# Kernel optimization log

Hardware: AMD Instinct MI355X
Metric: run time of the kernel (lower is better)

## Reference

```python
import jax, jax.numpy as jnp
import numpy as np

# Model hyperparameters (from __init__)
SIGMA = 0.2
LAMBDA_0 = 1.0
LAMBDA_INF = 0.1
LAMBDA_DECAY = 0.01
MU_J = 0.0
SIGMA_J = 0.3
TOTAL_STEPS = 10000
KAPPA = float(np.exp(MU_J + 0.5 * SIGMA_J ** 2) - 1.0)  # E[e^Y - 1]

# Simulation dims (simulate_path args)
T_TOTAL = 1.0
N_STEPS = 2048
N_PATHS = 32768
DT = T_TOTAL / N_STEPS


def _jump_intensity(t):
    # lambda(t) = lambda_inf + (lambda_0 - lambda_inf) * exp(-decay * t)
    # (t/total_steps * total_steps cancels in the original code)
    return LAMBDA_INF + (LAMBDA_0 - LAMBDA_INF) * jnp.exp(-LAMBDA_DECAY * t)


def setup_inputs() -> dict:
    key = jax.random.key(0)
    k1, k2, k3 = jax.random.split(key, 3)
    # Per-step time-varying Poisson rate for jump counts
    t = jnp.arange(N_STEPS, dtype=jnp.float32) * DT  # (n_steps,)
    lam_dt = _jump_intensity(t) * DT                  # (n_steps,)
    n_jumps = jax.random.poisson(k3, lam_dt[:, None], shape=(N_STEPS, N_PATHS)).astype(jnp.int32)
    return {
        "S0": jnp.ones((1,), dtype=jnp.float32),                         # initial price
        "z_diff": jax.random.normal(k1, (N_STEPS, N_PATHS), jnp.float32),  # Brownian increments / sqrt(dt)
        "z_jump": jax.random.normal(k2, (N_STEPS, N_PATHS), jnp.float32),  # jump-sum normals
        "n_jumps": n_jumps,                                              # Poisson jump counts
    }


def reference(S0, z_diff, z_jump, n_jumps):
    dtype = z_diff.dtype
    t = jnp.arange(N_STEPS, dtype=dtype) * DT          # (n_steps,)
    lam = _jump_intensity(t)[:, None]                   # (n_steps, 1)
    # Sum of n_jumps iid N(mu_J, sigma_J^2) jumps == N(n*mu_J, n*sigma_J^2)
    nj = n_jumps.astype(dtype)
    jump_sizes = nj * MU_J + jnp.sqrt(nj) * SIGMA_J * z_jump
    drift = (0.0 - lam * KAPPA) * DT
    diffusion = SIGMA * jnp.asarray(np.sqrt(DT), dtype) * z_diff
    log_ret = drift + diffusion + jump_sizes            # (n_steps, n_paths)
    log_paths = jnp.cumsum(log_ret, axis=0)             # (n_steps, n_paths)
    log_paths = jnp.concatenate([jnp.zeros((1, log_ret.shape[1]), dtype), log_paths], axis=0)
    paths = (S0[0] * jnp.exp(log_paths)).T              # (n_paths, n_steps + 1)
    return paths
```

## Files before the change

kernel.cpp:

```cpp
#include <hip/hip_runtime.h>
#include <math.h>


#define N_STEPS 2048
#define N_PATHS 32768
#define U 16
#define TILE_S 64
#define ROW (N_STEPS + 1)

#define DT_F 0.00048828125f
#define C_DIFF_F 0.004419417382415922f
#define KAPPA_F 0.046027859908717f

__device__ __forceinline__ void load_batch(const float* __restrict__ zd_p,
                                           const float* __restrict__ zj_p,
                                           const int* __restrict__ nj_p,
                                           int base, float* zd, float* zj, int* nj) {
#pragma unroll
    for (int i = 0; i < U; ++i) {
        int off = (base + i) * N_PATHS;
        zd[i] = zd_p[off];
        zj[i] = zj_p[off];
        nj[i] = nj_p[off];
    }
}

__device__ __forceinline__ void compute_batch(int jbase, const float* zd, const float* zj,
                                              const int* nj, float& acc, float& e,
                                              float r, float s0,
                                              float* __restrict__ smem_row) {
#pragma unroll
    for (int i = 0; i < U; ++i) {
        float lam = 0.1f + 0.9f * e;
        e *= r;
        float drift = -(lam * KAPPA_F) * DT_F;
        float njf = (float)nj[i];
        float val = (drift + C_DIFF_F * zd[i]) + sqrtf(njf) * 0.3f * zj[i];
        acc += val;
        smem_row[jbase + i] = s0 * __expf(acc);
    }
}

__global__ __launch_bounds__(64) void merton_paths_kernel(
    const float* __restrict__ S0,
    const float* __restrict__ z_diff,
    const float* __restrict__ z_jump,
    const int* __restrict__ n_jumps,
    float* __restrict__ out) {
    const int lane = threadIdx.x;
    const int pbase = blockIdx.x * 64;
    const int p = pbase + lane;
    const float s0 = S0[0];

    __shared__ float smem[64][TILE_S + 1];

    const float* zd_p = z_diff + p;
    const float* zj_p = z_jump + p;
    const int* nj_p = n_jumps + p;

    out[(long)p * ROW] = s0;

    float zdA[U], zjA[U]; int njA[U];
    float zdB[U], zjB[U]; int njB[U];

    float acc = 0.0f;
    float e = 1.0f;
    const float r = __expf(-0.01f * DT_F);

    load_batch(zd_p, zj_p, nj_p, 0, zdA, zjA, njA);

    for (int tb = 0; tb < N_STEPS; tb += TILE_S) {
        load_batch(zd_p, zj_p, nj_p, tb + U, zdB, zjB, njB);
        compute_batch(0, zdA, zjA, njA, acc, e, r, s0, smem[lane]);
        load_batch(zd_p, zj_p, nj_p, tb + 2 * U, zdA, zjA, njA);
        compute_batch(U, zdB, zjB, njB, acc, e, r, s0, smem[lane]);
        load_batch(zd_p, zj_p, nj_p, tb + 3 * U, zdB, zjB, njB);
        compute_batch(2 * U, zdA, zjA, njA, acc, e, r, s0, smem[lane]);
        if (tb + TILE_S < N_STEPS)
            load_batch(zd_p, zj_p, nj_p, tb + TILE_S, zdA, zjA, njA);
        compute_batch(3 * U, zdB, zjB, njB, acc, e, r, s0, smem[lane]);

        __syncthreads();
        float* orow = out + (long)pbase * ROW + 1 + tb + lane;
#pragma unroll 16
        for (int rr = 0; rr < 64; ++rr) {
            *orow = smem[rr][lane];
            orow += ROW;
        }
        __syncthreads();
    }
}

extern "C" void kernel_launch(void* const* d_in, const int* in_sizes, int n_in,
                              void* d_out, int out_size, void* d_ws, size_t ws_size,
                              hipStream_t stream) {
    const float* S0      = (const float*)d_in[0];
    const float* z_diff  = (const float*)d_in[1];
    const float* z_jump  = (const float*)d_in[2];
    const int*   n_jumps = (const int*)d_in[3];
    float* out = (float*)d_out;

    dim3 block(64);
    dim3 grid(N_PATHS / 64);
    hipLaunchKernelGGL(merton_paths_kernel, grid, block, 0, stream,
                       S0, z_diff, z_jump, n_jumps, out);
}
```

Baseline: 879.1 us.

## Split time axis across 16 waves with block-level scan of path prefix sums

Each block now runs 16 waves instead of one. Each wave handles 8 consecutive time steps of a 128-step tile, and per-wave partial sums are combined through shared memory into a carried prefix, so one path's sequential cumsum is parallelized across waves. The intent is more memory-level parallelism and occupancy for a bandwidth-bound kernel, plus wider output stores of 128 contiguous floats per row. The cost is three barriers per tile, a recomputed exponential for the intensity, and a slightly different floating-point summation order.

Result: faster. 840.4 us (-4.4%).

```diff
diff --git a/kernel.cpp b/kernel.cpp
--- a/kernel.cpp
+++ b/kernel.cpp
@@ -4,90 +4,101 @@
 
 #define N_STEPS 2048
 #define N_PATHS 32768
-#define U 16
-#define TILE_S 64
 #define ROW (N_STEPS + 1)
+
+#define NWAVES 16
+#define SUB 8
+#define TILE_S (NWAVES * SUB)
+#define NTILES (N_STEPS / TILE_S)
 
 #define DT_F 0.00048828125f
 #define C_DIFF_F 0.004419417382415922f
 #define KAPPA_F 0.046027859908717f
+#define ND_F (-4.8828125e-6f)
 
-__device__ __forceinline__ void load_batch(const float* __restrict__ zd_p,
-                                           const float* __restrict__ zj_p,
-                                           const int* __restrict__ nj_p,
-                                           int base, float* zd, float* zj, int* nj) {
-#pragma unroll
-    for (int i = 0; i < U; ++i) {
-        int off = (base + i) * N_PATHS;
-        zd[i] = zd_p[off];
-        zj[i] = zj_p[off];
-        nj[i] = nj_p[off];
-    }
-}
-
-__device__ __forceinline__ void compute_batch(int jbase, const float* zd, const float* zj,
-                                              const int* nj, float& acc, float& e,
-                                              float r, float s0,
-                                              float* __restrict__ smem_row) {
-#pragma unroll
-    for (int i = 0; i < U; ++i) {
-        float lam = 0.1f + 0.9f * e;
-        e *= r;
-        float drift = -(lam * KAPPA_F) * DT_F;
-        float njf = (float)nj[i];
-        float val = (drift + C_DIFF_F * zd[i]) + sqrtf(njf) * 0.3f * zj[i];
-        acc += val;
-        smem_row[jbase + i] = s0 * __expf(acc);
-    }
-}
-
-__global__ __launch_bounds__(64) void merton_paths_kernel(
+__global__ __launch_bounds__(1024, 4) void merton_paths_kernel(
     const float* __restrict__ S0,
     const float* __restrict__ z_diff,
     const float* __restrict__ z_jump,
     const int* __restrict__ n_jumps,
     float* __restrict__ out) {
-    const int lane = threadIdx.x;
+    const int tid  = threadIdx.x;
+    const int lane = tid & 63;
+    const int w    = tid >> 6;
     const int pbase = blockIdx.x * 64;
-    const int p = pbase + lane;
-    const float s0 = S0[0];
+    const int p     = pbase + lane;
+    const float s0  = S0[0];
 
-    __shared__ float smem[64][TILE_S + 1];
+    __shared__ float stage[64][TILE_S + 1];
+    __shared__ float ws[NWAVES][64];
 
-    const float* zd_p = z_diff + p;
-    const float* zj_p = z_jump + p;
-    const int* nj_p = n_jumps + p;
+    const float r = __expf(ND_F);
 
-    out[(long)p * ROW] = s0;
+    if (w == 0) out[(size_t)p * ROW] = s0;
 
-    float zdA[U], zjA[U]; int njA[U];
-    float zdB[U], zjB[U]; int njB[U];
+    const float* zd_p = z_diff  + (size_t)(w * SUB) * N_PATHS + p;
+    const float* zj_p = z_jump  + (size_t)(w * SUB) * N_PATHS + p;
+    const int*   nj_p = n_jumps + (size_t)(w * SUB) * N_PATHS + p;
 
-    float acc = 0.0f;
-    float e = 1.0f;
-    const float r = __expf(-0.01f * DT_F);
+    float carry = 0.0f;
 
-    load_batch(zd_p, zj_p, nj_p, 0, zdA, zjA, njA);
+    for (int t = 0; t < NTILES; ++t) {
+        float zd[SUB], zj[SUB];
+        int   nj[SUB];
+#pragma unroll
+        for (int i = 0; i < SUB; ++i) {
+            size_t off = (size_t)i * N_PATHS;
+            zd[i] = zd_p[off];
+            zj[i] = zj_p[off];
+            nj[i] = nj_p[off];
+        }
+        float e = __expf(ND_F * (float)(t * TILE_S + w * SUB));
+        float c[SUB];
+        float acc = 0.0f;
+#pragma unroll
+        for (int i = 0; i < SUB; ++i) {
+            float lam = 0.1f + 0.9f * e;
+            e *= r;
+            float drift = -(lam * KAPPA_F) * DT_F;
+            float njf = (float)nj[i];
+            float val = (drift + C_DIFF_F * zd[i]) + sqrtf(njf) * 0.3f * zj[i];
+            acc += val;
+            c[i] = acc;
+        }
+        ws[w][lane] = acc;
+        __syncthreads();
 
-    for (int tb = 0; tb < N_STEPS; tb += TILE_S) {
-        load_batch(zd_p, zj_p, nj_p, tb + U, zdB, zjB, njB);
-        compute_batch(0, zdA, zjA, njA, acc, e, r, s0, smem[lane]);
-        load_batch(zd_p, zj_p, nj_p, tb + 2 * U, zdA, zjA, njA);
-        compute_batch(U, zdB, zjB, njB, acc, e, r, s0, smem[lane]);
-        load_batch(zd_p, zj_p, nj_p, tb + 3 * U, zdB, zjB, njB);
-        compute_batch(2 * U, zdA, zjA, njA, acc, e, r, s0, smem[lane]);
-        if (tb + TILE_S < N_STEPS)
-            load_batch(zd_p, zj_p, nj_p, tb + TILE_S, zdA, zjA, njA);
-        compute_batch(3 * U, zdB, zjB, njB, acc, e, r, s0, smem[lane]);
+        float pre = carry;
+        float tot = 0.0f;
+#pragma unroll
+        for (int ww = 0; ww < NWAVES; ++ww) {
+            float v = ws[ww][lane];
+            pre += (ww < w) ? v : 0.0f;
+            tot += v;
+        }
+        carry += tot;
 
-        __syncthreads();
-        float* orow = out + (long)pbase * ROW + 1 + tb + lane;
-#pragma unroll 16
-        for (int rr = 0; rr < 64; ++rr) {
-            *orow = smem[rr][lane];
-            orow += ROW;
+#pragma unroll
+        for (int i = 0; i < SUB; ++i) {
+            stage[lane][w * SUB + i] = s0 * __expf(pre + c[i]);
         }
         __syncthreads();
+
+        {
+            float* obase = out + (size_t)pbase * ROW + 1 + t * TILE_S;
+#pragma unroll
+            for (int k = 0; k < 4; ++k) {
+                int rr = w * 4 + k;
+                float* orow = obase + (size_t)rr * ROW;
+                orow[lane]      = stage[rr][lane];
+                orow[lane + 64] = stage[rr][lane + 64];
+            }
+        }
+        __syncthreads();
+
+        zd_p += (size_t)TILE_S * N_PATHS;
+        zj_p += (size_t)TILE_S * N_PATHS;
+        nj_p += (size_t)TILE_S * N_PATHS;
     }
 }
 
@@ -100,7 +111,7 @@
     const int*   n_jumps = (const int*)d_in[3];
     float* out = (float*)d_out;
 
-    dim3 block(64);
+    dim3 block(1024);
     dim3 grid(N_PATHS / 64);
     hipLaunchKernelGGL(merton_paths_kernel, grid, block, 0, stream,
                        S0, z_diff, z_jump, n_jumps, out);
```
